# Kernel tuning notes

Measured on AMD Instinct MI355X. Metric: run time of the kernel, lower is better.

The kernel has to match this reference:

```python
import jax, jax.numpy as jnp
import numpy as np


def setup_inputs() -> dict:
    key = jax.random.key(0)
    k1, k2 = jax.random.split(key)
    N, D = 200000, 256
    B, S = 32768, 10  # batch of nodes, num_sample=10 (module default)
    features = jax.random.normal(k1, (N, D), dtype=jnp.float32)
    nbrs = jax.random.randint(k2, (B, S), 0, N, dtype=jnp.int64)
    return {"features": features, "nbrs": nbrs}


def reference(features, nbrs):
    # Faithful to MeanAggregator: mask is 0/1 over the SET of sampled
    # neighbors, so duplicate samples within a row count once. We weight
    # only the first occurrence of each index per row, then take the
    # weighted mean -- identical math to mask.div(num_neigh).mm(emb).
    B, S = nbrs.shape
    eq = nbrs[:, :, None] == nbrs[:, None, :]          # [B, S, S]
    earlier = jnp.tril(jnp.ones((S, S), dtype=bool), k=-1)  # j < i
    dup = jnp.any(eq & earlier[None], axis=2)          # [B, S] repeated entry
    w = jnp.where(dup, 0.0, 1.0).astype(features.dtype)  # [B, S]
    gathered = features[nbrs]                          # [B, S, D] gather
    num = jnp.einsum('bs,bsd->bd', w, gathered)        # sum over distinct nbrs
    den = jnp.sum(w, axis=1, keepdims=True)            # num_neigh per row
    return num / den
```

## Files before the change

### kernel.cpp

```cpp
#include <hip/hip_runtime.h>


#define AGG_S 10
#define AGG_D 256

typedef __attribute__((ext_vector_type(4))) float f32x4;

__global__ __launch_bounds__(256, 8) void MeanAggregator_58514634441194_kernel(
    const float* __restrict__ feat,
    const int* __restrict__ nbrs,
    float* __restrict__ out,
    int B)
{
    const int tid  = blockIdx.x * blockDim.x + threadIdx.x;
    const int lane = threadIdx.x & 63;
    const int wave = __builtin_amdgcn_readfirstlane(tid >> 6);
    if (wave >= B) return;

    const int* __restrict__ row = nbrs + (size_t)wave * AGG_S;
    int idx[AGG_S];
#pragma unroll
    for (int s = 0; s < AGG_S; ++s)
        idx[s] = __builtin_amdgcn_readfirstlane(row[s]);

    float w[AGG_S];
    float cnt = 0.0f;
#pragma unroll
    for (int s = 0; s < AGG_S; ++s) {
        bool dup = false;
#pragma unroll
        for (int j = 0; j < AGG_S; ++j) {
            if (j < s) dup |= (idx[j] == idx[s]);
        }
        w[s] = dup ? 0.0f : 1.0f;
        cnt += w[s];
    }

    float4 v[AGG_S];
#pragma unroll
    for (int s = 0; s < AGG_S; ++s) {
        const float4* __restrict__ p =
            (const float4*)(feat + (size_t)idx[s] * AGG_D);
        v[s] = p[lane];
    }

    float4 acc = make_float4(0.f, 0.f, 0.f, 0.f);
#pragma unroll
    for (int s = 0; s < AGG_S; ++s) {
        acc.x = fmaf(w[s], v[s].x, acc.x);
        acc.y = fmaf(w[s], v[s].y, acc.y);
        acc.z = fmaf(w[s], v[s].z, acc.z);
        acc.w = fmaf(w[s], v[s].w, acc.w);
    }

    const float inv = 1.0f / cnt;
    acc.x *= inv; acc.y *= inv; acc.z *= inv; acc.w *= inv;

    f32x4 accv;
    accv.x = acc.x; accv.y = acc.y; accv.z = acc.z; accv.w = acc.w;
    f32x4* __restrict__ dst = (f32x4*)(out + (size_t)wave * AGG_D) + lane;
    __builtin_nontemporal_store(accv, dst);
}

extern "C" void kernel_launch(void* const* d_in, const int* in_sizes, int n_in,
                              void* d_out, int out_size, void* d_ws, size_t ws_size,
                              hipStream_t stream)
{
    const float* feat = (const float*)d_in[0];
    const int*   nbrs = (const int*)d_in[1];
    float*       out  = (float*)d_out;

    const int B = in_sizes[1] / AGG_S;
    const int threads = 256;
    const int rows_per_block = threads / 64;
    const int blocks = (B + rows_per_block - 1) / rows_per_block;

    MeanAggregator_58514634441194_kernel<<<blocks, threads, 0, stream>>>(
        feat, nbrs, out, B);
}
```

Measured before the change: 287.2 us.

## Use grid-stride persistent waves and prefetch next row's neighbor indices

The launch is capped at 2048 blocks, and each wave now loops over rows with a grid stride instead of handling a single row. Inside the loop, the next row's neighbor indices are loaded after the current row's feature gathers are issued, which hides the dependent index-load latency. This is meant to remove per-wave launch and startup costs and the serialized load chain of index then gather. In exchange, fewer waves are in flight at once, and the loop-carried prefetch adds register pressure.

```diff
diff --git a/kernel.cpp b/kernel.cpp
--- a/kernel.cpp
+++ b/kernel.cpp
@@ -12,54 +12,72 @@
     float* __restrict__ out,
     int B)
 {
-    const int tid  = blockIdx.x * blockDim.x + threadIdx.x;
-    const int lane = threadIdx.x & 63;
-    const int wave = __builtin_amdgcn_readfirstlane(tid >> 6);
-    if (wave >= B) return;
+    const int lane  = threadIdx.x & 63;
+    const int wave0 = __builtin_amdgcn_readfirstlane(
+        (int)((blockIdx.x * blockDim.x + threadIdx.x) >> 6));
+    const int W     = __builtin_amdgcn_readfirstlane(
+        (int)((gridDim.x * blockDim.x) >> 6));
+    if (wave0 >= B) return;
 
-    const int* __restrict__ row = nbrs + (size_t)wave * AGG_S;
     int idx[AGG_S];
+    {
+        const int* __restrict__ row = nbrs + (size_t)wave0 * AGG_S;
 #pragma unroll
-    for (int s = 0; s < AGG_S; ++s)
-        idx[s] = __builtin_amdgcn_readfirstlane(row[s]);
-
-    float w[AGG_S];
-    float cnt = 0.0f;
-#pragma unroll
-    for (int s = 0; s < AGG_S; ++s) {
-        bool dup = false;
-#pragma unroll
-        for (int j = 0; j < AGG_S; ++j) {
-            if (j < s) dup |= (idx[j] == idx[s]);
-        }
-        w[s] = dup ? 0.0f : 1.0f;
-        cnt += w[s];
+        for (int s = 0; s < AGG_S; ++s)
+            idx[s] = __builtin_amdgcn_readfirstlane(row[s]);
     }
 
-    float4 v[AGG_S];
+    for (int r = wave0; r < B; r += W) {
+        float4 v[AGG_S];
 #pragma unroll
-    for (int s = 0; s < AGG_S; ++s) {
-        const float4* __restrict__ p =
-            (const float4*)(feat + (size_t)idx[s] * AGG_D);
-        v[s] = p[lane];
+        for (int s = 0; s < AGG_S; ++s) {
+            const float4* __restrict__ p =
+                (const float4*)(feat + (size_t)idx[s] * AGG_D);
+            v[s] = p[lane];
+        }
+
+        const int rn = (r + W < B) ? (r + W) : r;
+        int nidx[AGG_S];
+        {
+            const int* __restrict__ nrow = nbrs + (size_t)rn * AGG_S;
+#pragma unroll
+            for (int s = 0; s < AGG_S; ++s)
+                nidx[s] = __builtin_amdgcn_readfirstlane(nrow[s]);
+        }
+
+        float w[AGG_S];
+        float cnt = 0.0f;
+#pragma unroll
+        for (int s = 0; s < AGG_S; ++s) {
+            bool dup = false;
+#pragma unroll
+            for (int j = 0; j < AGG_S; ++j) {
+                if (j < s) dup |= (idx[j] == idx[s]);
+            }
+            w[s] = dup ? 0.0f : 1.0f;
+            cnt += w[s];
+        }
+
+        float4 acc = make_float4(0.f, 0.f, 0.f, 0.f);
+#pragma unroll
+        for (int s = 0; s < AGG_S; ++s) {
+            acc.x = fmaf(w[s], v[s].x, acc.x);
+            acc.y = fmaf(w[s], v[s].y, acc.y);
+            acc.z = fmaf(w[s], v[s].z, acc.z);
+            acc.w = fmaf(w[s], v[s].w, acc.w);
+        }
+
+        const float inv = 1.0f / cnt;
+        acc.x *= inv; acc.y *= inv; acc.z *= inv; acc.w *= inv;
+
+        f32x4 accv;
+        accv.x = acc.x; accv.y = acc.y; accv.z = acc.z; accv.w = acc.w;
+        f32x4* __restrict__ dst = (f32x4*)(out + (size_t)r * AGG_D) + lane;
+        __builtin_nontemporal_store(accv, dst);
+
+#pragma unroll
+        for (int s = 0; s < AGG_S; ++s) idx[s] = nidx[s];
     }
-
-    float4 acc = make_float4(0.f, 0.f, 0.f, 0.f);
-#pragma unroll
-    for (int s = 0; s < AGG_S; ++s) {
-        acc.x = fmaf(w[s], v[s].x, acc.x);
-        acc.y = fmaf(w[s], v[s].y, acc.y);
-        acc.z = fmaf(w[s], v[s].z, acc.z);
-        acc.w = fmaf(w[s], v[s].w, acc.w);
-    }
-
-    const float inv = 1.0f / cnt;
-    acc.x *= inv; acc.y *= inv; acc.z *= inv; acc.w *= inv;
-
-    f32x4 accv;
-    accv.x = acc.x; accv.y = acc.y; accv.z = acc.z; accv.w = acc.w;
-    f32x4* __restrict__ dst = (f32x4*)(out + (size_t)wave * AGG_D) + lane;
-    __builtin_nontemporal_store(accv, dst);
 }
 
 extern "C" void kernel_launch(void* const* d_in, const int* in_sizes, int n_in,
@@ -72,8 +90,10 @@
 
     const int B = in_sizes[1] / AGG_S;
     const int threads = 256;
+    int blocks = 2048;
     const int rows_per_block = threads / 64;
-    const int blocks = (B + rows_per_block - 1) / rows_per_block;
+    const int max_blocks = (B + rows_per_block - 1) / rows_per_block;
+    if (blocks > max_blocks) blocks = max_blocks;
 
     MeanAggregator_58514634441194_kernel<<<blocks, threads, 0, stream>>>(
         feat, nbrs, out, B);
```

New measurement: 290.1 us. Within noise of the previous version (+1.0%).
